# Performance work log

Measured on AMD Instinct MI355X. Metric: run time of the kernel, lower is better.

Reference implementation:

```python
import jax, jax.numpy as jnp
import numpy as np

# Photon library / detector geometry constants
NX, NY, NZ = 64, 64, 64          # voxel grid
N_VOX = NX * NY * NZ             # 262,144 voxels
N_PMT = 180                      # number of PMTs (columns of vis LUT)
N_CLUSTERS = 128                 # number of charge clusters (= len(dx))
PTS_PER_CLUSTER = 8192
TOTAL = N_CLUSTERS * PTS_PER_CLUSTER  # 1,048,576 charge points
LOWER = jnp.array([0.0, 0.0, 0.0], dtype=jnp.float32)
VOXEL_SIZE = jnp.array([1.0, 1.0, 1.0], dtype=jnp.float32)


def coord_to_voxel(coords):
    """Uniform-grid voxelization; x is the fastest-varying index so that
    vox_id + 1 is the neighbor voxel along x (matches the original backward)."""
    idx = jnp.floor((coords - LOWER) / VOXEL_SIZE).astype(jnp.int32)
    idx = jnp.clip(idx, 0, jnp.array([NX - 1, NY - 1, NZ - 1], dtype=jnp.int32))
    return idx[:, 0] + NX * (idx[:, 1] + NY * idx[:, 2])


def setup_inputs() -> dict:
    key = jax.random.key(0)
    k1, k2, k3, k4 = jax.random.split(key, 4)
    # coords: x in [8, 56) so dx in [-5, 5] stays in-grid; y,z in [0, 64)
    xyz = jax.random.uniform(
        k1, (TOTAL, 3),
        minval=jnp.array([8.0, 0.0, 0.0]),
        maxval=jnp.array([56.0, 64.0, 64.0]),
        dtype=jnp.float32,
    )
    q = jax.random.uniform(k2, (TOTAL, 1), dtype=jnp.float32)  # charge > 0
    batch = jnp.concatenate([xyz, q], axis=1)  # [TOTAL, 4]
    sizes = jnp.full((N_CLUSTERS,), PTS_PER_CLUSTER, dtype=jnp.int32)
    dx = jax.random.uniform(k3, (N_CLUSTERS,), minval=-3.0, maxval=3.0,
                            dtype=jnp.float32)
    dx_ranges = jnp.stack(
        [jnp.full((N_CLUSTERS,), -5.0, dtype=jnp.float32),
         jnp.full((N_CLUSTERS,), 5.0, dtype=jnp.float32)], axis=1)
    vis = jax.random.uniform(k4, (N_VOX, N_PMT), dtype=jnp.float32) * 1e-3
    return {"dx": dx, "batch": batch, "sizes": sizes,
            "dx_ranges": dx_ranges, "vis": vis}


def reference(dx, batch, sizes, dx_ranges, vis):
    # mask_dx(clamp=True): clamp per-cluster offsets to their ranges
    dx_c = jnp.clip(dx, dx_ranges[:, 0], dx_ranges[:, 1])  # [N_CLUSTERS]
    # cluster id per point (torch.repeat_interleave / torch.split equivalent)
    seg = jnp.repeat(jnp.arange(N_CLUSTERS, dtype=jnp.int32), sizes,
                     total_repeat_length=TOTAL)  # [TOTAL]
    coords = batch[:, :3].at[:, 0].add(dx_c[seg])  # shift x per cluster
    q = batch[:, 3]
    vox_ids = coord_to_voxel(coords)               # [TOTAL] int32
    vis_q = vis[vox_ids] * q[:, None]              # [TOTAL, N_PMT] gather+scale
    # ragged per-cluster sum (torch.split + per-segment sum, fused)
    pred = jax.ops.segment_sum(vis_q, seg, num_segments=N_CLUSTERS)
    return pred  # [N_CLUSTERS, N_PMT]
```

## Files before the change

### kernel.cpp

```cpp
#include <hip/hip_runtime.h>

#define N_PMT 180
#define N_PMT4 45
#define N_CLUSTERS 128
#define BPC 16
#define BLOCK 256
#define NWAVE (BLOCK / 64)
#define MLP 8


__global__ void prep_kernel(const float* __restrict__ dx,
                            const int* __restrict__ sizes,
                            const float* __restrict__ dx_ranges,
                            int* __restrict__ offsets,
                            float* __restrict__ dxc) {
    __shared__ int s[N_CLUSTERS];
    const int t = threadIdx.x;
    s[t] = sizes[t];
    float lo = dx_ranges[2 * t];
    float hi = dx_ranges[2 * t + 1];
    dxc[t] = fminf(fmaxf(dx[t], lo), hi);
    __syncthreads();
    int acc = 0;
    for (int i = 0; i < t; ++i) acc += s[i];
    offsets[t] = acc;
    if (t == N_CLUSTERS - 1) offsets[N_CLUSTERS] = acc + s[t];
}

__global__ __launch_bounds__(BLOCK) void gather_kernel(
    const float4* __restrict__ batch,
    const float4* __restrict__ vis4,
    const int*    __restrict__ offsets,
    const float*  __restrict__ dxc,
    float* __restrict__ out) {

    const int b     = blockIdx.x;
    const int c     = b / BPC;
    const int sub   = b % BPC;
    const int start = offsets[c];
    const int end   = offsets[c + 1];
    const int count = end - start;
    const int chunk = (count + BPC - 1) / BPC;
    const int s0 = start + sub * chunk;
    const int s1 = min(s0 + chunk, end);

    const int wave = threadIdx.x >> 6;
    const int lane = threadIdx.x & 63;

    const int wtotal = s1 - s0;
    const int per = (wtotal + NWAVE - 1) / NWAVE;
    const int ws0 = s0 + wave * per;
    const int ws1 = min(ws0 + per, s1);

    const float dxc_c = dxc[c];
    const bool active = (lane < N_PMT4);

    float4 accE = {0.f, 0.f, 0.f, 0.f};
    float4 accO = {0.f, 0.f, 0.f, 0.f};

    for (int base = ws0; base < ws1; base += 64) {
        const int p = base + lane;
        float q = 0.f;
        int vox = 0;
        if (p < ws1) {
            float4 pd = batch[p];
            float x = pd.x + dxc_c;
            int ix = (int)floorf(x);
            int iy = (int)floorf(pd.y);
            int iz = (int)floorf(pd.z);
            ix = max(0, min(63, ix));
            iy = max(0, min(63, iy));
            iz = max(0, min(63, iz));
            vox = ix + 64 * (iy + 64 * iz);
            q = pd.w;
        }
        #pragma unroll
        for (int j0 = 0; j0 < 64; j0 += MLP) {
            float4 r[MLP];
            float  qs[MLP];
            #pragma unroll
            for (int jj = 0; jj < MLP; ++jj)
                qs[jj] = __uint_as_float(
                    __builtin_amdgcn_readlane(__float_as_uint(q), j0 + jj));
            if (active) {
                #pragma unroll
                for (int jj = 0; jj < MLP; ++jj) {
                    const int v = __builtin_amdgcn_readlane(vox, j0 + jj);
                    r[jj] = vis4[(size_t)v * N_PMT4 + lane];
                }
                #pragma unroll
                for (int jj = 0; jj < MLP; ++jj) {
                    const float qq = qs[jj];
                    if (jj & 1) {
                        accO.x = fmaf(r[jj].x, qq, accO.x);
                        accO.y = fmaf(r[jj].y, qq, accO.y);
                        accO.z = fmaf(r[jj].z, qq, accO.z);
                        accO.w = fmaf(r[jj].w, qq, accO.w);
                    } else {
                        accE.x = fmaf(r[jj].x, qq, accE.x);
                        accE.y = fmaf(r[jj].y, qq, accE.y);
                        accE.z = fmaf(r[jj].z, qq, accE.z);
                        accE.w = fmaf(r[jj].w, qq, accE.w);
                    }
                }
            }
        }
    }

    __shared__ float sacc[N_PMT];
    for (int i = threadIdx.x; i < N_PMT; i += BLOCK) sacc[i] = 0.f;
    __syncthreads();
    if (active) {
        atomicAdd(&sacc[lane * 4 + 0], accE.x + accO.x);
        atomicAdd(&sacc[lane * 4 + 1], accE.y + accO.y);
        atomicAdd(&sacc[lane * 4 + 2], accE.z + accO.z);
        atomicAdd(&sacc[lane * 4 + 3], accE.w + accO.w);
    }
    __syncthreads();
    for (int i = threadIdx.x; i < N_PMT; i += BLOCK)
        atomicAdd(&out[c * N_PMT + i], sacc[i]);
}

extern "C" void kernel_launch(void* const* d_in, const int* in_sizes, int n_in,
                              void* d_out, int out_size, void* d_ws, size_t ws_size,
                              hipStream_t stream) {
    const float* dx        = (const float*)d_in[0];
    const float* batch     = (const float*)d_in[1];
    const int*   sizes     = (const int*)d_in[2];
    const float* dx_ranges = (const float*)d_in[3];
    const float* vis       = (const float*)d_in[4];
    float* out = (float*)d_out;

    int*   offsets = (int*)d_ws;
    float* dxc     = (float*)((char*)d_ws + sizeof(int) * (N_CLUSTERS + 1));

    hipMemsetAsync(out, 0, (size_t)out_size * sizeof(float), stream);

    prep_kernel<<<1, N_CLUSTERS, 0, stream>>>(dx, sizes, dx_ranges, offsets, dxc);

    gather_kernel<<<N_CLUSTERS * BPC, BLOCK, 0, stream>>>(
        (const float4*)batch, (const float4*)vis, offsets, dxc, out);
}
```

Measured before the change: 347.1 us.

## Voxelize and bucket-sort points per cluster before gathering vis rows

Adds a voxelize kernel that writes (voxel, charge) pairs, then a per-cluster counting sort on the high voxel bits (z and upper y) so that nearby voxels are gathered together, improving cache locality of the vis LUT reads. The gather kernel then reads the sorted pairs and replaces the per-block shared atomics with a per-wave shared reduction, interleaving cluster blocks across the grid. This adds two extra kernels and 16 bytes per point of workspace traffic. The old path is kept as a fallback when the workspace is too small, and that fallback was simplified to single-load unrolling.

New measurement: 340.7 us. Within noise of the previous version (-1.9%).

```diff
diff --git a/kernel.cpp b/kernel.cpp
--- a/kernel.cpp
+++ b/kernel.cpp
@@ -3,6 +3,7 @@
 #define N_PMT 180
 #define N_PMT4 45
 #define N_CLUSTERS 128
+#define NBINS 512
 #define BPC 16
 #define BLOCK 256
 #define NWAVE (BLOCK / 64)
@@ -12,7 +13,7 @@
 __global__ void prep_kernel(const float* __restrict__ dx,
                             const int* __restrict__ sizes,
                             const float* __restrict__ dx_ranges,
-                            int* __restrict__ offsets,
+                            int* __restrict__ offsC,
                             float* __restrict__ dxc) {
     __shared__ int s[N_CLUSTERS];
     const int t = threadIdx.x;
@@ -23,8 +24,129 @@
     __syncthreads();
     int acc = 0;
     for (int i = 0; i < t; ++i) acc += s[i];
-    offsets[t] = acc;
-    if (t == N_CLUSTERS - 1) offsets[N_CLUSTERS] = acc + s[t];
+    offsC[t] = acc;
+    if (t == N_CLUSTERS - 1) offsC[N_CLUSTERS] = acc + s[t];
+}
+
+__global__ void k1_voxelize(const float4* __restrict__ batch,
+                            const int* __restrict__ offsC,
+                            const float* __restrict__ dxc,
+                            int n, uint2* __restrict__ vq) {
+    int i = blockIdx.x * 256 + threadIdx.x;
+    if (i >= n) return;
+    int lo = 0, hi = N_CLUSTERS - 1;
+    #pragma unroll
+    for (int s = 0; s < 7; ++s) {
+        int mid = (lo + hi + 1) >> 1;
+        if (i >= offsC[mid]) lo = mid; else hi = mid - 1;
+    }
+    float4 pd = batch[i];
+    int ix = max(0, min(63, (int)floorf(pd.x + dxc[lo])));
+    int iy = max(0, min(63, (int)floorf(pd.y)));
+    int iz = max(0, min(63, (int)floorf(pd.z)));
+    vq[i] = make_uint2((unsigned)(ix + 64 * (iy + 64 * iz)), __float_as_uint(pd.w));
+}
+
+__global__ __launch_bounds__(1024) void ksort(const int* __restrict__ offsC,
+                                              const uint2* __restrict__ vq,
+                                              uint2* __restrict__ sorted) {
+    __shared__ int hist[NBINS], sa[NBINS], sb[NBINS], cur[NBINS];
+    const int c = blockIdx.x, t = threadIdx.x;
+    const int e0 = offsC[c], e1 = offsC[c + 1], cnt = e1 - e0;
+    if (t < NBINS) hist[t] = 0;
+    __syncthreads();
+    for (int i = t; i < cnt; i += 1024)
+        atomicAdd(&hist[vq[e0 + i].x >> 9], 1);
+    __syncthreads();
+    if (t < NBINS) sa[t] = hist[t];
+    __syncthreads();
+    int* src = sa; int* dst = sb;
+    for (int d = 1; d < NBINS; d <<= 1) {
+        if (t < NBINS) dst[t] = src[t] + (t >= d ? src[t - d] : 0);
+        __syncthreads();
+        int* tmp = src; src = dst; dst = tmp;
+    }
+    if (t < NBINS) cur[t] = src[t] - hist[t];
+    __syncthreads();
+    for (int i = t; i < cnt; i += 1024) {
+        uint2 e = vq[e0 + i];
+        int pos = atomicAdd(&cur[e.x >> 9], 1);
+        sorted[e0 + pos] = e;
+    }
+}
+
+__global__ __launch_bounds__(BLOCK) void k_gather(
+    const uint2*  __restrict__ sorted,
+    const float4* __restrict__ vis4,
+    const int*    __restrict__ offsC,
+    float* __restrict__ out) {
+
+    const int c   = blockIdx.x & (N_CLUSTERS - 1);
+    const int sub = blockIdx.x >> 7;
+    const int start = offsC[c], end = offsC[c + 1];
+    const int count = end - start;
+    const int chunk = (count + BPC - 1) / BPC;
+    const int s0 = start + sub * chunk;
+    const int s1 = min(s0 + chunk, end);
+
+    const int wave = threadIdx.x >> 6, lane = threadIdx.x & 63;
+    const int wtotal = s1 - s0;
+    const int per = (wtotal + NWAVE - 1) / NWAVE;
+    const int ws0 = s0 + wave * per;
+    const int ws1 = min(ws0 + per, s1);
+
+    const int lclamp = min(lane, N_PMT4 - 1);
+
+    float4 accE = {0.f, 0.f, 0.f, 0.f};
+    float4 accO = {0.f, 0.f, 0.f, 0.f};
+
+    for (int base = ws0; base < ws1; base += 64) {
+        const int p = base + lane;
+        uint2 se = (p < ws1) ? sorted[p] : make_uint2(0u, 0u);
+        const int   vox = (int)se.x;
+        const float q   = __uint_as_float(se.y);
+        #pragma unroll
+        for (int j0 = 0; j0 < 64; j0 += MLP) {
+            int vs[MLP]; float qs[MLP]; float4 r[MLP];
+            #pragma unroll
+            for (int jj = 0; jj < MLP; ++jj) {
+                vs[jj] = __builtin_amdgcn_readlane(vox, j0 + jj);
+                qs[jj] = __uint_as_float(
+                    __builtin_amdgcn_readlane(__float_as_uint(q), j0 + jj));
+            }
+            #pragma unroll
+            for (int jj = 0; jj < MLP; ++jj)
+                r[jj] = vis4[(size_t)vs[jj] * N_PMT4 + lclamp];
+            #pragma unroll
+            for (int jj = 0; jj < MLP; ++jj) {
+                const float qq = qs[jj];
+                if (jj & 1) {
+                    accO.x = fmaf(r[jj].x, qq, accO.x);
+                    accO.y = fmaf(r[jj].y, qq, accO.y);
+                    accO.z = fmaf(r[jj].z, qq, accO.z);
+                    accO.w = fmaf(r[jj].w, qq, accO.w);
+                } else {
+                    accE.x = fmaf(r[jj].x, qq, accE.x);
+                    accE.y = fmaf(r[jj].y, qq, accE.y);
+                    accE.z = fmaf(r[jj].z, qq, accE.z);
+                    accE.w = fmaf(r[jj].w, qq, accE.w);
+                }
+            }
+        }
+    }
+
+    __shared__ float sacc[NWAVE][184];
+    if (lane < N_PMT4) {
+        sacc[wave][lane * 4 + 0] = accE.x + accO.x;
+        sacc[wave][lane * 4 + 1] = accE.y + accO.y;
+        sacc[wave][lane * 4 + 2] = accE.z + accO.z;
+        sacc[wave][lane * 4 + 3] = accE.w + accO.w;
+    }
+    __syncthreads();
+    for (int i = threadIdx.x; i < N_PMT; i += BLOCK) {
+        float s = sacc[0][i] + sacc[1][i] + sacc[2][i] + sacc[3][i];
+        atomicAdd(&out[c * N_PMT + i], s);
+    }
 }
 
 __global__ __launch_bounds__(BLOCK) void gather_kernel(
@@ -33,88 +155,53 @@
     const int*    __restrict__ offsets,
     const float*  __restrict__ dxc,
     float* __restrict__ out) {
-
-    const int b     = blockIdx.x;
-    const int c     = b / BPC;
-    const int sub   = b % BPC;
-    const int start = offsets[c];
-    const int end   = offsets[c + 1];
+    const int b = blockIdx.x;
+    const int c = b / BPC, sub = b % BPC;
+    const int start = offsets[c], end = offsets[c + 1];
     const int count = end - start;
     const int chunk = (count + BPC - 1) / BPC;
     const int s0 = start + sub * chunk;
     const int s1 = min(s0 + chunk, end);
-
-    const int wave = threadIdx.x >> 6;
-    const int lane = threadIdx.x & 63;
-
+    const int wave = threadIdx.x >> 6, lane = threadIdx.x & 63;
     const int wtotal = s1 - s0;
     const int per = (wtotal + NWAVE - 1) / NWAVE;
     const int ws0 = s0 + wave * per;
     const int ws1 = min(ws0 + per, s1);
-
     const float dxc_c = dxc[c];
     const bool active = (lane < N_PMT4);
-
     float4 accE = {0.f, 0.f, 0.f, 0.f};
-    float4 accO = {0.f, 0.f, 0.f, 0.f};
-
     for (int base = ws0; base < ws1; base += 64) {
         const int p = base + lane;
-        float q = 0.f;
-        int vox = 0;
+        float q = 0.f; int vox = 0;
         if (p < ws1) {
             float4 pd = batch[p];
-            float x = pd.x + dxc_c;
-            int ix = (int)floorf(x);
-            int iy = (int)floorf(pd.y);
-            int iz = (int)floorf(pd.z);
-            ix = max(0, min(63, ix));
-            iy = max(0, min(63, iy));
-            iz = max(0, min(63, iz));
+            int ix = max(0, min(63, (int)floorf(pd.x + dxc_c)));
+            int iy = max(0, min(63, (int)floorf(pd.y)));
+            int iz = max(0, min(63, (int)floorf(pd.z)));
             vox = ix + 64 * (iy + 64 * iz);
             q = pd.w;
         }
         #pragma unroll
-        for (int j0 = 0; j0 < 64; j0 += MLP) {
-            float4 r[MLP];
-            float  qs[MLP];
-            #pragma unroll
-            for (int jj = 0; jj < MLP; ++jj)
-                qs[jj] = __uint_as_float(
-                    __builtin_amdgcn_readlane(__float_as_uint(q), j0 + jj));
+        for (int j = 0; j < 64; ++j) {
+            const int   v  = __builtin_amdgcn_readlane(vox, j);
+            const float qj = __uint_as_float(__builtin_amdgcn_readlane(__float_as_uint(q), j));
             if (active) {
-                #pragma unroll
-                for (int jj = 0; jj < MLP; ++jj) {
-                    const int v = __builtin_amdgcn_readlane(vox, j0 + jj);
-                    r[jj] = vis4[(size_t)v * N_PMT4 + lane];
-                }
-                #pragma unroll
-                for (int jj = 0; jj < MLP; ++jj) {
-                    const float qq = qs[jj];
-                    if (jj & 1) {
-                        accO.x = fmaf(r[jj].x, qq, accO.x);
-                        accO.y = fmaf(r[jj].y, qq, accO.y);
-                        accO.z = fmaf(r[jj].z, qq, accO.z);
-                        accO.w = fmaf(r[jj].w, qq, accO.w);
-                    } else {
-                        accE.x = fmaf(r[jj].x, qq, accE.x);
-                        accE.y = fmaf(r[jj].y, qq, accE.y);
-                        accE.z = fmaf(r[jj].z, qq, accE.z);
-                        accE.w = fmaf(r[jj].w, qq, accE.w);
-                    }
-                }
+                float4 r = vis4[(size_t)v * N_PMT4 + lane];
+                accE.x = fmaf(r.x, qj, accE.x);
+                accE.y = fmaf(r.y, qj, accE.y);
+                accE.z = fmaf(r.z, qj, accE.z);
+                accE.w = fmaf(r.w, qj, accE.w);
             }
         }
     }
-
     __shared__ float sacc[N_PMT];
     for (int i = threadIdx.x; i < N_PMT; i += BLOCK) sacc[i] = 0.f;
     __syncthreads();
     if (active) {
-        atomicAdd(&sacc[lane * 4 + 0], accE.x + accO.x);
-        atomicAdd(&sacc[lane * 4 + 1], accE.y + accO.y);
-        atomicAdd(&sacc[lane * 4 + 2], accE.z + accO.z);
-        atomicAdd(&sacc[lane * 4 + 3], accE.w + accO.w);
+        atomicAdd(&sacc[lane * 4 + 0], accE.x);
+        atomicAdd(&sacc[lane * 4 + 1], accE.y);
+        atomicAdd(&sacc[lane * 4 + 2], accE.z);
+        atomicAdd(&sacc[lane * 4 + 3], accE.w);
     }
     __syncthreads();
     for (int i = threadIdx.x; i < N_PMT; i += BLOCK)
@@ -130,14 +217,26 @@
     const float* dx_ranges = (const float*)d_in[3];
     const float* vis       = (const float*)d_in[4];
     float* out = (float*)d_out;
-
-    int*   offsets = (int*)d_ws;
-    float* dxc     = (float*)((char*)d_ws + sizeof(int) * (N_CLUSTERS + 1));
+    char*  wsb = (char*)d_ws;
+    const int n = in_sizes[1] / 4;
+
+    int*   offsC  = (int*)(wsb + 0);
+    float* dxc    = (float*)(wsb + 1024);
+    uint2* vq     = (uint2*)(wsb + 2048);
+    uint2* sorted = (uint2*)(wsb + 2048 + (size_t)8 * n);
 
     hipMemsetAsync(out, 0, (size_t)out_size * sizeof(float), stream);
-
-    prep_kernel<<<1, N_CLUSTERS, 0, stream>>>(dx, sizes, dx_ranges, offsets, dxc);
-
-    gather_kernel<<<N_CLUSTERS * BPC, BLOCK, 0, stream>>>(
-        (const float4*)batch, (const float4*)vis, offsets, dxc, out);
-}
+    prep_kernel<<<1, N_CLUSTERS, 0, stream>>>(dx, sizes, dx_ranges, offsC, dxc);
+
+    const size_t need = 2048ull + 16ull * (size_t)n;
+    if (ws_size >= need) {
+        k1_voxelize<<<(n + 255) / 256, 256, 0, stream>>>(
+            (const float4*)batch, offsC, dxc, n, vq);
+        ksort<<<N_CLUSTERS, 1024, 0, stream>>>(offsC, vq, sorted);
+        k_gather<<<N_CLUSTERS * BPC, BLOCK, 0, stream>>>(
+            sorted, (const float4*)vis, offsC, out);
+    } else {
+        gather_kernel<<<N_CLUSTERS * BPC, BLOCK, 0, stream>>>(
+            (const float4*)batch, (const float4*)vis, offsC, dxc, out);
+    }
+}
```
